# Performance work log

Measured on AMD Instinct MI355X. Metric: run time of the kernel, lower is better.

## Reference

```python
import jax, jax.numpy as jnp
import numpy as np

MAX_LEN = 512   # static padding cap for the ragged sequences
EPS = 1e-12     # F.normalize default eps


def setup_inputs() -> dict:
    key = jax.random.key(0)
    ks = jax.random.split(key, 6)
    B, T, D, H = 2048, 262144, 64, 128
    x = jax.random.normal(ks[0], (T, D), jnp.float32)
    offsets = jnp.sort(jax.random.randint(ks[1], (B,), 0, T)).astype(jnp.int64)
    offsets = offsets.at[0].set(0)  # first segment starts at 0 as in EmbeddingLookup
    W_ih = jax.random.normal(ks[2], (3 * H, D), jnp.float32) * 0.1   # [r,z,n] stacked
    W_hh = jax.random.normal(ks[3], (3 * H, H), jnp.float32) * 0.1
    W_dense = jax.random.normal(ks[4], (D, H), jnp.float32) * 0.1
    b_dense = jax.random.normal(ks[5], (D,), jnp.float32) * 0.1
    return {"x": x, "offsets": offsets, "W_ih": W_ih, "W_hh": W_hh,
            "W_dense": W_dense, "b_dense": b_dense}


def _forward(x, W_ih, W_hh, W_dense, b_dense, offsets):
    T, D = x.shape
    B = offsets.shape[0]
    H = W_hh.shape[1]
    # segment lengths as in get_field_embedding_list: diffs + trailing segment
    lengths = jnp.concatenate([offsets[1:] - offsets[:-1], T - offsets[-1:]])
    lengths = jnp.clip(lengths, 1, MAX_LEN)
    # ragged -> padded [B, L, D] (pad_sequence equivalent)
    t_idx = jnp.arange(MAX_LEN)
    gidx = jnp.clip(offsets[:, None] + t_idx[None, :], 0, T - 1)      # [B, L]
    mask = (t_idx[None, :] < lengths[:, None]).astype(x.dtype)        # [B, L]
    padded = x[gidx] * mask[:, :, None]                               # [B, L, D]
    # single-layer GRU, bias=False, batch_first; scan over time
    xs = jnp.transpose(padded, (1, 0, 2))                             # [L, B, D]

    def step(h, x_t):
        gi = x_t @ W_ih.T                                             # [B, 3H]
        gh = h @ W_hh.T                                               # [B, 3H]
        ir, iz, inn = jnp.split(gi, 3, axis=-1)
        hr, hz, hn = jnp.split(gh, 3, axis=-1)
        r = jax.nn.sigmoid(ir + hr)
        z = jax.nn.sigmoid(iz + hz)
        n = jnp.tanh(inn + r * hn)
        h_new = (1.0 - z) * n + z * h
        return h_new, h_new

    h0 = jnp.zeros((B, H), x.dtype)
    _, ys = jax.lax.scan(step, h0, xs)                                # [L, B, H]
    gru_out = jnp.transpose(ys, (1, 0, 2))                            # [B, L, H]
    # gather_indexes: hidden state at last valid timestep
    last = gru_out[jnp.arange(B), lengths - 1]                        # [B, H]
    out = last @ W_dense.T + b_dense                                  # [B, D]
    norm = jnp.linalg.norm(out, axis=-1, keepdims=True)
    return out / jnp.maximum(norm, EPS)


def reference(x, offsets, W_ih, W_hh, W_dense, b_dense):
    return _forward(x, W_ih, W_hh, W_dense, b_dense, offsets)
```

## Files before the change

kernel.cpp:

```cpp
#include <hip/hip_runtime.h>
#include <math.h>

constexpr int D = 64;
constexpr int H = 128;
constexpr int MAXLEN = 512;
constexpr int MSEQ = 16;

typedef __attribute__((ext_vector_type(8))) short short8;
typedef __attribute__((ext_vector_type(4))) float f32x4;

__device__ __forceinline__ short f2bf(float f) {
    unsigned u = __float_as_uint(f);
    u += 0x7fffu + ((u >> 16) & 1u);
    return (short)(u >> 16);
}
__device__ __forceinline__ unsigned cvtpk(float a, float b) {
    unsigned r;
    asm volatile("v_cvt_pk_bf16_f32 %0, %1, %2" : "=v"(r) : "v"(a), "v"(b));
    return r;
}
__device__ __forceinline__ short8 pack8(float4 a, float4 b) {
    short8 r;
    r[0]=f2bf(a.x); r[1]=f2bf(a.y); r[2]=f2bf(a.z); r[3]=f2bf(a.w);
    r[4]=f2bf(b.x); r[5]=f2bf(b.y); r[6]=f2bf(b.z); r[7]=f2bf(b.w);
    return r;
}
__device__ __forceinline__ float rcp_(float x) { return __builtin_amdgcn_rcpf(x); }
__device__ __forceinline__ float sig_(float v) { return rcp_(1.0f + __expf(-v)); }
__device__ __forceinline__ float tanh_(float v) {
    float a = fabsf(v);
    float e = __expf(2.0f * a);
    float t = 1.0f - 2.0f * rcp_(e + 1.0f);
    return copysignf(t, v);
}

__device__ __forceinline__ void lgkm_barrier() {
    asm volatile("s_waitcnt lgkmcnt(0)\n\ts_barrier" ::: "memory");
}

#define MFMA(a,b,c) __builtin_amdgcn_mfma_f32_16x16x32_bf16((a),(b),(c),0,0,0)

__global__ __launch_bounds__(512, 2)
void gru_mfma8(const float* __restrict__ x,
               const int* __restrict__ offsets,
               const float* __restrict__ W_ih,
               const float* __restrict__ W_hh,
               const float* __restrict__ W_dense,
               const float* __restrict__ b_dense,
               float* __restrict__ out,
               int B, int T)
{
    const int bb  = blockIdx.x;
    const int tid = threadIdx.x;
    const int w   = tid >> 6;
    const int l   = tid & 63;
    const int s   = l & 15;
    const int q   = l >> 4;
    const int sw  = s & 7;

    __shared__ __align__(16) short h_bf[2][MSEQ * H];
    __shared__ __align__(16) short x_bf[2][MSEQ * D];
    __shared__ int slen[MSEQ], sstart[MSEQ];
    __shared__ float h_f32[MSEQ][H];

    if (tid < MSEQ) {
        int sg = bb * MSEQ + tid;
        int st = 0, en = 1;
        if (sg < B) { st = offsets[sg]; en = (sg + 1 < B) ? offsets[sg + 1] : T; }
        int ln = en - st;
        ln = max(1, min(ln, MAXLEN));
        sstart[tid] = st; slen[tid] = ln;
    }
    {
        int* hz = (int*)h_bf[0];
        hz[tid] = 0; hz[tid + 512] = 0;
    }
    __syncthreads();

    int nt = 1;
#pragma unroll
    for (int i = 0; i < MSEQ; ++i) nt = max(nt, slen[i]);

    short8 Wh[3][4];
    short8 Wi[3][2];
#pragma unroll
    for (int g = 0; g < 3; ++g) {
        const int grow = g * H + w * 16 + s;
        const float* ph = W_hh + (size_t)grow * H + q * 8;
#pragma unroll
        for (int kt = 0; kt < 4; ++kt)
            Wh[g][kt] = pack8(*(const float4*)(ph + kt * 32),
                              *(const float4*)(ph + kt * 32 + 4));
        const float* pi = W_ih + (size_t)grow * D + q * 8;
#pragma unroll
        for (int kt = 0; kt < 2; ++kt)
            Wi[g][kt] = pack8(*(const float4*)(pi + kt * 32),
                              *(const float4*)(pi + kt * 32 + 4));
    }

    int hoff[4], xoff[2];
#pragma unroll
    for (int kt = 0; kt < 4; ++kt) hoff[kt] = s * 256 + (((kt * 4 + q) ^ sw) << 4);
#pragma unroll
    for (int kt = 0; kt < 2; ++kt) xoff[kt] = s * 128 + (((kt * 4 + q) ^ sw) << 4);
    const int woff = s * 256 + ((((2 * w) + (q >> 1)) ^ sw) << 4) + ((q & 1) << 3);

    const int ss  = tid >> 5;
    const int pxx = tid & 31;
    const int st_s = sstart[ss];
    const int ln_s = slen[ss];
    const float* xg = x + (size_t)st_s * D + pxx * 2;
    const int xwoff = ss * 128 + ((((pxx >> 2) ^ (ss & 7)) << 4)) + ((pxx & 3) << 2);

    {
        float2 v = *(const float2*)xg;
        *(unsigned*)((char*)x_bf[0] + xwoff) = cvtpk(v.x, v.y);
    }
    float2 xpf = *(const float2*)(xg + (size_t)min(1, ln_s - 1) * D);

    const int lenS = slen[s];
    float hreg[4] = {0.f, 0.f, 0.f, 0.f};

    __syncthreads();

    for (int t = 0; t < nt; ++t) {
        const int p = t & 1;
        const char* hb = (const char*)h_bf[p];
        const char* xb = (const char*)x_bf[p];

        short8 bh[4], bx[2];
#pragma unroll
        for (int kt = 0; kt < 4; ++kt) bh[kt] = *(const short8*)(hb + hoff[kt]);
#pragma unroll
        for (int kt = 0; kt < 2; ++kt) bx[kt] = *(const short8*)(xb + xoff[kt]);

        const int tn = (t + 2 < ln_s) ? t + 2 : ln_s - 1;
        float2 xnew = *(const float2*)(xg + (size_t)tn * D);

        f32x4 cr = {0,0,0,0}, cz = {0,0,0,0}, ci = {0,0,0,0}, chh = {0,0,0,0};
#pragma unroll
        for (int kt = 0; kt < 2; ++kt) {
            cr = MFMA(Wi[0][kt], bx[kt], cr);
            cz = MFMA(Wi[1][kt], bx[kt], cz);
            ci = MFMA(Wi[2][kt], bx[kt], ci);
        }
#pragma unroll
        for (int kt = 0; kt < 4; ++kt) {
            cr  = MFMA(Wh[0][kt], bh[kt], cr);
            cz  = MFMA(Wh[1][kt], bh[kt], cz);
            chh = MFMA(Wh[2][kt], bh[kt], chh);
        }

        const bool upd = (t < lenS);
#pragma unroll
        for (int j = 0; j < 4; ++j) {
            float r  = sig_(cr[j]);
            float z  = sig_(cz[j]);
            float n  = tanh_(ci[j] + r * chh[j]);
            float hn = (1.0f - z) * n + z * hreg[j];
            hreg[j] = upd ? hn : hreg[j];
        }

        {
            char* hw = (char*)h_bf[p ^ 1];
            uint2 pr = { cvtpk(hreg[0], hreg[1]), cvtpk(hreg[2], hreg[3]) };
            *(uint2*)(hw + woff) = pr;
            *(unsigned*)((char*)x_bf[p ^ 1] + xwoff) = cvtpk(xpf.x, xpf.y);
        }
        xpf = xnew;

        lgkm_barrier();
    }

    {
        float4 hv = { hreg[0], hreg[1], hreg[2], hreg[3] };
        *(float4*)&h_f32[s][w * 16 + q * 4] = hv;
    }
    __syncthreads();

    {
        const int s2 = tid >> 5;
        const int cb = tid & 31;
        float acc0 = b_dense[cb];
        float acc1 = b_dense[cb + 32];
        const float* w0 = W_dense + (size_t)cb * H;
        const float* w1 = W_dense + (size_t)(cb + 32) * H;
#pragma unroll
        for (int j = 0; j < H; j += 4) {
            float4 hv = *(const float4*)&h_f32[s2][j];
            float4 a0 = *(const float4*)(w0 + j);
            float4 a1 = *(const float4*)(w1 + j);
            acc0 += hv.x*a0.x + hv.y*a0.y + hv.z*a0.z + hv.w*a0.w;
            acc1 += hv.x*a1.x + hv.y*a1.y + hv.z*a1.z + hv.w*a1.w;
        }
        float s2q = acc0 * acc0 + acc1 * acc1;
#pragma unroll
        for (int off = 16; off >= 1; off >>= 1) s2q += __shfl_xor(s2q, off);
        float invn = 1.0f / fmaxf(sqrtf(s2q), 1e-12f);
        int sg = bb * MSEQ + s2;
        if (sg < B) {
            out[(size_t)sg * D + cb]      = acc0 * invn;
            out[(size_t)sg * D + cb + 32] = acc1 * invn;
        }
    }
}

extern "C" void kernel_launch(void* const* d_in, const int* in_sizes, int n_in,
                              void* d_out, int out_size, void* d_ws, size_t ws_size,
                              hipStream_t stream) {
    const float* x       = (const float*)d_in[0];
    const int*   offsets = (const int*)d_in[1];
    const float* W_ih    = (const float*)d_in[2];
    const float* W_hh    = (const float*)d_in[3];
    const float* W_dense = (const float*)d_in[4];
    const float* b_dense = (const float*)d_in[5];
    float*       out     = (float*)d_out;

    const int B = in_sizes[1];
    const int T = in_sizes[0] / D;
    const int grid = (B + MSEQ - 1) / MSEQ;

    gru_mfma8<<<grid, 512, 0, stream>>>(x, offsets, W_ih, W_hh, W_dense, b_dense, out, B, T);
}
```

Baseline: 398.8 us.

## Halve sequences per block and load x directly into MFMA registers

Each block now handles 8 sequences instead of 16, which doubles the grid so more blocks run the latency-bound recurrence concurrently. The 16-wide MFMA N dimension is filled by duplicating the 8 sequences, and each lane keeps only half of the accumulator outputs. The x input is loaded from global memory straight into bf16 MFMA fragments with a two-step register prefetch, which removes the shared-memory x staging buffer. Tanh is also rewritten as a single sigmoid-style expression, and the dense epilogue now uses one output column per thread. This wastes half of the MFMA work and issues more, redundant global loads of x.

```diff
diff --git a/kernel.cpp b/kernel.cpp
--- a/kernel.cpp
+++ b/kernel.cpp
@@ -4,7 +4,7 @@
 constexpr int D = 64;
 constexpr int H = 128;
 constexpr int MAXLEN = 512;
-constexpr int MSEQ = 16;
+constexpr int MSEQ = 8;
 
 typedef __attribute__((ext_vector_type(8))) short short8;
 typedef __attribute__((ext_vector_type(4))) float f32x4;
@@ -25,13 +25,16 @@
     r[4]=f2bf(b.x); r[5]=f2bf(b.y); r[6]=f2bf(b.z); r[7]=f2bf(b.w);
     return r;
 }
+__device__ __forceinline__ short8 cvt8(float4 a, float4 b) {
+    union { unsigned u[4]; short8 s; } r;
+    r.u[0] = cvtpk(a.x, a.y); r.u[1] = cvtpk(a.z, a.w);
+    r.u[2] = cvtpk(b.x, b.y); r.u[3] = cvtpk(b.z, b.w);
+    return r.s;
+}
 __device__ __forceinline__ float rcp_(float x) { return __builtin_amdgcn_rcpf(x); }
 __device__ __forceinline__ float sig_(float v) { return rcp_(1.0f + __expf(-v)); }
 __device__ __forceinline__ float tanh_(float v) {
-    float a = fabsf(v);
-    float e = __expf(2.0f * a);
-    float t = 1.0f - 2.0f * rcp_(e + 1.0f);
-    return copysignf(t, v);
+    return fmaf(2.0f, rcp_(1.0f + __expf(-2.0f * v)), -1.0f);
 }
 
 __device__ __forceinline__ void lgkm_barrier() {
@@ -41,14 +44,14 @@
 #define MFMA(a,b,c) __builtin_amdgcn_mfma_f32_16x16x32_bf16((a),(b),(c),0,0,0)
 
 __global__ __launch_bounds__(512, 2)
-void gru_mfma8(const float* __restrict__ x,
-               const int* __restrict__ offsets,
-               const float* __restrict__ W_ih,
-               const float* __restrict__ W_hh,
-               const float* __restrict__ W_dense,
-               const float* __restrict__ b_dense,
-               float* __restrict__ out,
-               int B, int T)
+void gru_mfma8s(const float* __restrict__ x,
+                const int* __restrict__ offsets,
+                const float* __restrict__ W_ih,
+                const float* __restrict__ W_hh,
+                const float* __restrict__ W_dense,
+                const float* __restrict__ b_dense,
+                float* __restrict__ out,
+                int B, int T)
 {
     const int bb  = blockIdx.x;
     const int tid = threadIdx.x;
@@ -56,10 +59,10 @@
     const int l   = tid & 63;
     const int s   = l & 15;
     const int q   = l >> 4;
-    const int sw  = s & 7;
+    const int sq  = s & 7;
+    const bool hi = (s >= 8);
 
     __shared__ __align__(16) short h_bf[2][MSEQ * H];
-    __shared__ __align__(16) short x_bf[2][MSEQ * D];
     __shared__ int slen[MSEQ], sstart[MSEQ];
     __shared__ float h_f32[MSEQ][H];
 
@@ -71,10 +74,7 @@
         ln = max(1, min(ln, MAXLEN));
         sstart[tid] = st; slen[tid] = ln;
     }
-    {
-        int* hz = (int*)h_bf[0];
-        hz[tid] = 0; hz[tid + 512] = 0;
-    }
+    ((int*)h_bf[0])[tid] = 0;
     __syncthreads();
 
     int nt = 1;
@@ -98,51 +98,54 @@
                               *(const float4*)(pi + kt * 32 + 4));
     }
 
-    int hoff[4], xoff[2];
-#pragma unroll
-    for (int kt = 0; kt < 4; ++kt) hoff[kt] = s * 256 + (((kt * 4 + q) ^ sw) << 4);
-#pragma unroll
-    for (int kt = 0; kt < 2; ++kt) xoff[kt] = s * 128 + (((kt * 4 + q) ^ sw) << 4);
-    const int woff = s * 256 + ((((2 * w) + (q >> 1)) ^ sw) << 4) + ((q & 1) << 3);
-
-    const int ss  = tid >> 5;
-    const int pxx = tid & 31;
-    const int st_s = sstart[ss];
-    const int ln_s = slen[ss];
-    const float* xg = x + (size_t)st_s * D + pxx * 2;
-    const int xwoff = ss * 128 + ((((pxx >> 2) ^ (ss & 7)) << 4)) + ((pxx & 3) << 2);
-
+    int hoff[4];
+#pragma unroll
+    for (int kt = 0; kt < 4; ++kt) hoff[kt] = sq * 256 + (((kt * 4 + q) ^ sq) << 4);
+    const int woff = sq * 256 + ((((2 * w) + (q >> 1)) ^ sq) << 4)
+                   + ((q & 1) << 3) + (hi ? 4 : 0);
+
+    const int st_s = sstart[sq];
+    const int ln_s = slen[sq];
+    const float* xg = x + (size_t)st_s * D + q * 8;
+
+    short8 bxc[2];
     {
-        float2 v = *(const float2*)xg;
-        *(unsigned*)((char*)x_bf[0] + xwoff) = cvtpk(v.x, v.y);
-    }
-    float2 xpf = *(const float2*)(xg + (size_t)min(1, ln_s - 1) * D);
-
-    const int lenS = slen[s];
-    float hreg[4] = {0.f, 0.f, 0.f, 0.f};
+        float4 a0 = *(const float4*)(xg);
+        float4 a1 = *(const float4*)(xg + 4);
+        float4 a2 = *(const float4*)(xg + 32);
+        float4 a3 = *(const float4*)(xg + 36);
+        bxc[0] = cvt8(a0, a1); bxc[1] = cvt8(a2, a3);
+    }
+    const size_t r1 = (size_t)min(1, ln_s - 1) * D;
+    float4 rb0 = *(const float4*)(xg + r1);
+    float4 rb1 = *(const float4*)(xg + r1 + 4);
+    float4 rb2 = *(const float4*)(xg + r1 + 32);
+    float4 rb3 = *(const float4*)(xg + r1 + 36);
+
+    float h0 = 0.f, h1 = 0.f;
 
     __syncthreads();
 
     for (int t = 0; t < nt; ++t) {
         const int p = t & 1;
         const char* hb = (const char*)h_bf[p];
-        const char* xb = (const char*)x_bf[p];
-
-        short8 bh[4], bx[2];
+
+        short8 bh[4];
 #pragma unroll
         for (int kt = 0; kt < 4; ++kt) bh[kt] = *(const short8*)(hb + hoff[kt]);
-#pragma unroll
-        for (int kt = 0; kt < 2; ++kt) bx[kt] = *(const short8*)(xb + xoff[kt]);
-
-        const int tn = (t + 2 < ln_s) ? t + 2 : ln_s - 1;
-        float2 xnew = *(const float2*)(xg + (size_t)tn * D);
+
+        const size_t rn = (size_t)((t + 2 < ln_s) ? t + 2 : ln_s - 1) * D;
+        float4 rc0 = *(const float4*)(xg + rn);
+        float4 rc1 = *(const float4*)(xg + rn + 4);
+        float4 rc2 = *(const float4*)(xg + rn + 32);
+        float4 rc3 = *(const float4*)(xg + rn + 36);
 
         f32x4 cr = {0,0,0,0}, cz = {0,0,0,0}, ci = {0,0,0,0}, chh = {0,0,0,0};
 #pragma unroll
         for (int kt = 0; kt < 2; ++kt) {
-            cr = MFMA(Wi[0][kt], bx[kt], cr);
-            cz = MFMA(Wi[1][kt], bx[kt], cz);
-            ci = MFMA(Wi[2][kt], bx[kt], ci);
+            cr = MFMA(Wi[0][kt], bxc[kt], cr);
+            cz = MFMA(Wi[1][kt], bxc[kt], cz);
+            ci = MFMA(Wi[2][kt], bxc[kt], ci);
         }
 #pragma unroll
         for (int kt = 0; kt < 4; ++kt) {
@@ -151,57 +154,55 @@
             chh = MFMA(Wh[2][kt], bh[kt], chh);
         }
 
-        const bool upd = (t < lenS);
-#pragma unroll
-        for (int j = 0; j < 4; ++j) {
-            float r  = sig_(cr[j]);
-            float z  = sig_(cz[j]);
-            float n  = tanh_(ci[j] + r * chh[j]);
-            float hn = (1.0f - z) * n + z * hreg[j];
-            hreg[j] = upd ? hn : hreg[j];
-        }
-
         {
-            char* hw = (char*)h_bf[p ^ 1];
-            uint2 pr = { cvtpk(hreg[0], hreg[1]), cvtpk(hreg[2], hreg[3]) };
-            *(uint2*)(hw + woff) = pr;
-            *(unsigned*)((char*)x_bf[p ^ 1] + xwoff) = cvtpk(xpf.x, xpf.y);
-        }
-        xpf = xnew;
+            float vr0 = hi ? cr[2]  : cr[0],  vr1 = hi ? cr[3]  : cr[1];
+            float vz0 = hi ? cz[2]  : cz[0],  vz1 = hi ? cz[3]  : cz[1];
+            float vi0 = hi ? ci[2]  : ci[0],  vi1 = hi ? ci[3]  : ci[1];
+            float vh0 = hi ? chh[2] : chh[0], vh1 = hi ? chh[3] : chh[1];
+            float r0 = sig_(vr0), r1 = sig_(vr1);
+            float z0 = sig_(vz0), z1 = sig_(vz1);
+            float n0 = tanh_(vi0 + r0 * vh0);
+            float n1 = tanh_(vi1 + r1 * vh1);
+            float hn0 = (1.0f - z0) * n0 + z0 * h0;
+            float hn1 = (1.0f - z1) * n1 + z1 * h1;
+            const bool upd = (t < ln_s);
+            h0 = upd ? hn0 : h0;
+            h1 = upd ? hn1 : h1;
+        }
+
+        *(unsigned*)((char*)h_bf[p ^ 1] + woff) = cvtpk(h0, h1);
+
+        bxc[0] = cvt8(rb0, rb1); bxc[1] = cvt8(rb2, rb3);
+        rb0 = rc0; rb1 = rc1; rb2 = rc2; rb3 = rc3;
 
         lgkm_barrier();
     }
 
     {
-        float4 hv = { hreg[0], hreg[1], hreg[2], hreg[3] };
-        *(float4*)&h_f32[s][w * 16 + q * 4] = hv;
+        float2 hv = { h0, h1 };
+        *(float2*)&h_f32[sq][w * 16 + q * 4 + (hi ? 2 : 0)] = hv;
     }
     __syncthreads();
 
     {
-        const int s2 = tid >> 5;
-        const int cb = tid & 31;
-        float acc0 = b_dense[cb];
-        float acc1 = b_dense[cb + 32];
-        const float* w0 = W_dense + (size_t)cb * H;
-        const float* w1 = W_dense + (size_t)(cb + 32) * H;
+        const int s2 = tid >> 6;
+        const int cb = tid & 63;
+        float acc = b_dense[cb];
+        const float* wd = W_dense + (size_t)cb * H;
+        float a0=0.f,a1=0.f,a2=0.f,a3=0.f;
 #pragma unroll
         for (int j = 0; j < H; j += 4) {
             float4 hv = *(const float4*)&h_f32[s2][j];
-            float4 a0 = *(const float4*)(w0 + j);
-            float4 a1 = *(const float4*)(w1 + j);
-            acc0 += hv.x*a0.x + hv.y*a0.y + hv.z*a0.z + hv.w*a0.w;
-            acc1 += hv.x*a1.x + hv.y*a1.y + hv.z*a1.z + hv.w*a1.w;
-        }
-        float s2q = acc0 * acc0 + acc1 * acc1;
-#pragma unroll
-        for (int off = 16; off >= 1; off >>= 1) s2q += __shfl_xor(s2q, off);
+            float4 wv = *(const float4*)(wd + j);
+            a0 += hv.x*wv.x; a1 += hv.y*wv.y; a2 += hv.z*wv.z; a3 += hv.w*wv.w;
+        }
+        acc += (a0 + a1) + (a2 + a3);
+        float s2q = acc * acc;
+#pragma unroll
+        for (int off = 32; off >= 1; off >>= 1) s2q += __shfl_xor(s2q, off);
         float invn = 1.0f / fmaxf(sqrtf(s2q), 1e-12f);
         int sg = bb * MSEQ + s2;
-        if (sg < B) {
-            out[(size_t)sg * D + cb]      = acc0 * invn;
-            out[(size_t)sg * D + cb + 32] = acc1 * invn;
-        }
+        if (sg < B) out[(size_t)sg * D + cb] = acc * invn;
     }
 }
 
@@ -220,5 +221,5 @@
     const int T = in_sizes[0] / D;
     const int grid = (B + MSEQ - 1) / MSEQ;
 
-    gru_mfma8<<<grid, 512, 0, stream>>>(x, offsets, W_ih, W_hh, W_dense, b_dense, out, B, T);
-}
+    gru_mfma8s<<<grid, 512, 0, stream>>>(x, offsets, W_ih, W_hh, W_dense, b_dense, out, B, T);
+}
```

Measured after the change: 467.3 us. 1.17x slower.

## Halve sequences per block and use four waves covering two gate tiles each

Applied to the files above, without the earlier changes.

Each block now handles 8 sequences with 256 threads instead of 16 sequences with 512 threads, so the grid doubles and more CUs get a block. Each wave now computes two 16-row gate tiles, which doubles its MFMA count per timestep. The 16-column MFMA B operand duplicates the 8 sequences, so half of the matrix work is redundant. Each lane selects half of the accumulator outputs for the elementwise gate math and writes two packed bf16 pairs per step. The aim is to trade longer per-step MFMA chains for fewer waves per barrier and better CU coverage.

```diff
diff --git a/kernel.cpp b/kernel.cpp
--- a/kernel.cpp
+++ b/kernel.cpp
@@ -4,7 +4,7 @@
 constexpr int D = 64;
 constexpr int H = 128;
 constexpr int MAXLEN = 512;
-constexpr int MSEQ = 16;
+constexpr int MSEQ = 8;
 
 typedef __attribute__((ext_vector_type(8))) short short8;
 typedef __attribute__((ext_vector_type(4))) float f32x4;
@@ -33,30 +33,30 @@
     float t = 1.0f - 2.0f * rcp_(e + 1.0f);
     return copysignf(t, v);
 }
-
 __device__ __forceinline__ void lgkm_barrier() {
     asm volatile("s_waitcnt lgkmcnt(0)\n\ts_barrier" ::: "memory");
 }
 
 #define MFMA(a,b,c) __builtin_amdgcn_mfma_f32_16x16x32_bf16((a),(b),(c),0,0,0)
 
-__global__ __launch_bounds__(512, 2)
-void gru_mfma8(const float* __restrict__ x,
-               const int* __restrict__ offsets,
-               const float* __restrict__ W_ih,
-               const float* __restrict__ W_hh,
-               const float* __restrict__ W_dense,
-               const float* __restrict__ b_dense,
-               float* __restrict__ out,
-               int B, int T)
+__global__ __launch_bounds__(256, 1)
+void gru_w4(const float* __restrict__ x,
+            const int* __restrict__ offsets,
+            const float* __restrict__ W_ih,
+            const float* __restrict__ W_hh,
+            const float* __restrict__ W_dense,
+            const float* __restrict__ b_dense,
+            float* __restrict__ out,
+            int B, int T)
 {
-    const int bb  = blockIdx.x;
-    const int tid = threadIdx.x;
-    const int w   = tid >> 6;
-    const int l   = tid & 63;
-    const int s   = l & 15;
-    const int q   = l >> 4;
-    const int sw  = s & 7;
+    const int bb   = blockIdx.x;
+    const int tid  = threadIdx.x;
+    const int w    = tid >> 6;
+    const int l    = tid & 63;
+    const int s    = l & 15;
+    const int q    = l >> 4;
+    const int sq   = s & 7;
+    const int hsel = s >> 3;
 
     __shared__ __align__(16) short h_bf[2][MSEQ * H];
     __shared__ __align__(16) short x_bf[2][MSEQ * D];
@@ -73,7 +73,7 @@
     }
     {
         int* hz = (int*)h_bf[0];
-        hz[tid] = 0; hz[tid + 512] = 0;
+        hz[tid] = 0; hz[tid + 256] = 0;
     }
     __syncthreads();
 
@@ -81,45 +81,52 @@
 #pragma unroll
     for (int i = 0; i < MSEQ; ++i) nt = max(nt, slen[i]);
 
-    short8 Wh[3][4];
-    short8 Wi[3][2];
+    short8 Wh[3][2][4];
+    short8 Wi[3][2][2];
 #pragma unroll
     for (int g = 0; g < 3; ++g) {
-        const int grow = g * H + w * 16 + s;
-        const float* ph = W_hh + (size_t)grow * H + q * 8;
-#pragma unroll
-        for (int kt = 0; kt < 4; ++kt)
-            Wh[g][kt] = pack8(*(const float4*)(ph + kt * 32),
-                              *(const float4*)(ph + kt * 32 + 4));
-        const float* pi = W_ih + (size_t)grow * D + q * 8;
-#pragma unroll
-        for (int kt = 0; kt < 2; ++kt)
-            Wi[g][kt] = pack8(*(const float4*)(pi + kt * 32),
-                              *(const float4*)(pi + kt * 32 + 4));
-    }
-
-    int hoff[4], xoff[2];
-#pragma unroll
-    for (int kt = 0; kt < 4; ++kt) hoff[kt] = s * 256 + (((kt * 4 + q) ^ sw) << 4);
-#pragma unroll
-    for (int kt = 0; kt < 2; ++kt) xoff[kt] = s * 128 + (((kt * 4 + q) ^ sw) << 4);
-    const int woff = s * 256 + ((((2 * w) + (q >> 1)) ^ sw) << 4) + ((q & 1) << 3);
+#pragma unroll
+        for (int u = 0; u < 2; ++u) {
+            const int grow = g * H + w * 32 + u * 16 + s;
+            const float* ph = W_hh + (size_t)grow * H + q * 8;
+#pragma unroll
+            for (int kt = 0; kt < 4; ++kt)
+                Wh[g][u][kt] = pack8(*(const float4*)(ph + kt * 32),
+                                     *(const float4*)(ph + kt * 32 + 4));
+            const float* pi = W_ih + (size_t)grow * D + q * 8;
+#pragma unroll
+            for (int kt = 0; kt < 2; ++kt)
+                Wi[g][u][kt] = pack8(*(const float4*)(pi + kt * 32),
+                                     *(const float4*)(pi + kt * 32 + 4));
+        }
+    }
+
+    int hoff[4], xoff[2], woff[2];
+#pragma unroll
+    for (int kt = 0; kt < 4; ++kt) hoff[kt] = sq * 256 + (((kt * 4 + q) ^ sq) << 4);
+#pragma unroll
+    for (int kt = 0; kt < 2; ++kt) xoff[kt] = sq * 128 + (((kt * 4 + q) ^ sq) << 4);
+#pragma unroll
+    for (int u = 0; u < 2; ++u)
+        woff[u] = sq * 256 + ((((4 * w) + (2 * u) + (q >> 1)) ^ sq) << 4)
+                + ((q & 1) << 3) + (hsel << 2);
 
     const int ss  = tid >> 5;
     const int pxx = tid & 31;
-    const int st_s = sstart[ss];
-    const int ln_s = slen[ss];
-    const float* xg = x + (size_t)st_s * D + pxx * 2;
-    const int xwoff = ss * 128 + ((((pxx >> 2) ^ (ss & 7)) << 4)) + ((pxx & 3) << 2);
+    const int st_x = sstart[ss];
+    const int ln_x = slen[ss];
+    const float* xg = x + (size_t)st_x * D + pxx * 2;
+    const int xwoff = ss * 128 + (((pxx >> 2) ^ ss) << 4) + ((pxx & 3) << 2);
 
     {
         float2 v = *(const float2*)xg;
         *(unsigned*)((char*)x_bf[0] + xwoff) = cvtpk(v.x, v.y);
     }
-    float2 xpf = *(const float2*)(xg + (size_t)min(1, ln_s - 1) * D);
-
-    const int lenS = slen[s];
-    float hreg[4] = {0.f, 0.f, 0.f, 0.f};
+    float2 xpf = *(const float2*)(xg + (size_t)min(1, ln_x - 1) * D);
+
+    const int ln_s = slen[sq];
+    float h00 = 0.f, h01 = 0.f;
+    float h10 = 0.f, h11 = 0.f;
 
     __syncthreads();
 
@@ -134,47 +141,75 @@
 #pragma unroll
         for (int kt = 0; kt < 2; ++kt) bx[kt] = *(const short8*)(xb + xoff[kt]);
 
-        const int tn = (t + 2 < ln_s) ? t + 2 : ln_s - 1;
-        float2 xnew = *(const float2*)(xg + (size_t)tn * D);
-
-        f32x4 cr = {0,0,0,0}, cz = {0,0,0,0}, ci = {0,0,0,0}, chh = {0,0,0,0};
-#pragma unroll
-        for (int kt = 0; kt < 2; ++kt) {
-            cr = MFMA(Wi[0][kt], bx[kt], cr);
-            cz = MFMA(Wi[1][kt], bx[kt], cz);
-            ci = MFMA(Wi[2][kt], bx[kt], ci);
-        }
-#pragma unroll
-        for (int kt = 0; kt < 4; ++kt) {
-            cr  = MFMA(Wh[0][kt], bh[kt], cr);
-            cz  = MFMA(Wh[1][kt], bh[kt], cz);
-            chh = MFMA(Wh[2][kt], bh[kt], chh);
-        }
-
-        const bool upd = (t < lenS);
-#pragma unroll
-        for (int j = 0; j < 4; ++j) {
-            float r  = sig_(cr[j]);
-            float z  = sig_(cz[j]);
-            float n  = tanh_(ci[j] + r * chh[j]);
-            float hn = (1.0f - z) * n + z * hreg[j];
-            hreg[j] = upd ? hn : hreg[j];
-        }
-
+        float2 xnew;
         {
-            char* hw = (char*)h_bf[p ^ 1];
-            uint2 pr = { cvtpk(hreg[0], hreg[1]), cvtpk(hreg[2], hreg[3]) };
-            *(uint2*)(hw + woff) = pr;
-            *(unsigned*)((char*)x_bf[p ^ 1] + xwoff) = cvtpk(xpf.x, xpf.y);
-        }
+            const int tn = (t + 2 < ln_x) ? t + 2 : ln_x - 1;
+            xnew = *(const float2*)(xg + (size_t)tn * D);
+        }
+
+        f32x4 cr[2] = {{0,0,0,0},{0,0,0,0}};
+        f32x4 cz[2] = {{0,0,0,0},{0,0,0,0}};
+        f32x4 ci[2] = {{0,0,0,0},{0,0,0,0}};
+        f32x4 chh[2]= {{0,0,0,0},{0,0,0,0}};
+#pragma unroll
+        for (int u = 0; u < 2; ++u) {
+#pragma unroll
+            for (int kt = 0; kt < 2; ++kt) {
+                cr[u] = MFMA(Wi[0][u][kt], bx[kt], cr[u]);
+                cz[u] = MFMA(Wi[1][u][kt], bx[kt], cz[u]);
+                ci[u] = MFMA(Wi[2][u][kt], bx[kt], ci[u]);
+            }
+#pragma unroll
+            for (int kt = 0; kt < 4; ++kt) {
+                cr[u]  = MFMA(Wh[0][u][kt], bh[kt], cr[u]);
+                cz[u]  = MFMA(Wh[1][u][kt], bh[kt], cz[u]);
+                chh[u] = MFMA(Wh[2][u][kt], bh[kt], chh[u]);
+            }
+        }
+
+        const bool upd = (t < ln_s);
+        {
+            float vr0 = hsel ? cr[0][2]  : cr[0][0],  vr1 = hsel ? cr[0][3]  : cr[0][1];
+            float vz0 = hsel ? cz[0][2]  : cz[0][0],  vz1 = hsel ? cz[0][3]  : cz[0][1];
+            float vi0 = hsel ? ci[0][2]  : ci[0][0],  vi1 = hsel ? ci[0][3]  : ci[0][1];
+            float vh0 = hsel ? chh[0][2] : chh[0][0], vh1 = hsel ? chh[0][3] : chh[0][1];
+            float r0 = sig_(vr0), r1 = sig_(vr1);
+            float z0 = sig_(vz0), z1 = sig_(vz1);
+            float n0 = tanh_(vi0 + r0 * vh0);
+            float n1 = tanh_(vi1 + r1 * vh1);
+            float a0 = (1.0f - z0) * n0 + z0 * h00;
+            float a1 = (1.0f - z1) * n1 + z1 * h01;
+            h00 = upd ? a0 : h00;
+            h01 = upd ? a1 : h01;
+        }
+        {
+            float vr0 = hsel ? cr[1][2]  : cr[1][0],  vr1 = hsel ? cr[1][3]  : cr[1][1];
+            float vz0 = hsel ? cz[1][2]  : cz[1][0],  vz1 = hsel ? cz[1][3]  : cz[1][1];
+            float vi0 = hsel ? ci[1][2]  : ci[1][0],  vi1 = hsel ? ci[1][3]  : ci[1][1];
+            float vh0 = hsel ? chh[1][2] : chh[1][0], vh1 = hsel ? chh[1][3] : chh[1][1];
+            float r0 = sig_(vr0), r1 = sig_(vr1);
+            float z0 = sig_(vz0), z1 = sig_(vz1);
+            float n0 = tanh_(vi0 + r0 * vh0);
+            float n1 = tanh_(vi1 + r1 * vh1);
+            float a0 = (1.0f - z0) * n0 + z0 * h10;
+            float a1 = (1.0f - z1) * n1 + z1 * h11;
+            h10 = upd ? a0 : h10;
+            h11 = upd ? a1 : h11;
+        }
+
+        *(unsigned*)((char*)h_bf[p ^ 1] + woff[0]) = cvtpk(h00, h01);
+        *(unsigned*)((char*)h_bf[p ^ 1] + woff[1]) = cvtpk(h10, h11);
+        *(unsigned*)((char*)x_bf[p ^ 1] + xwoff)   = cvtpk(xpf.x, xpf.y);
         xpf = xnew;
 
         lgkm_barrier();
     }
 
     {
-        float4 hv = { hreg[0], hreg[1], hreg[2], hreg[3] };
-        *(float4*)&h_f32[s][w * 16 + q * 4] = hv;
+        float2 hv0 = { h00, h01 };
+        float2 hv1 = { h10, h11 };
+        *(float2*)&h_f32[sq][w * 32 + 0  + q * 4 + 2 * hsel] = hv0;
+        *(float2*)&h_f32[sq][w * 32 + 16 + q * 4 + 2 * hsel] = hv1;
     }
     __syncthreads();
 
@@ -220,5 +255,5 @@
     const int T = in_sizes[0] / D;
     const int grid = (B + MSEQ - 1) / MSEQ;
 
-    gru_mfma8<<<grid, 512, 0, stream>>>(x, offsets, W_ih, W_hh, W_dense, b_dense, out, B, T);
-}
+    gru_w4<<<grid, 256, 0, stream>>>(x, offsets, W_ih, W_hh, W_dense, b_dense, out, B, T);
+}
```

Result: faster. 352.6 us (-11.6%).
